# Kernel tuning notes

Hardware: AMD Instinct MI355X
Metric: run time of the kernel (lower is better)

Reference implementation:

```python
import jax, jax.numpy as jnp
import numpy as np
from jax import lax

INPUT_SIZE, HIDDEN, LAYERS, OUT = 49, 32, 2, 10
B, T = 512, 1024


def _param(key, shape, fan):
    bound = 1.0 / np.sqrt(fan)
    return jax.random.uniform(key, shape, jnp.float32, -bound, bound)


def setup_inputs() -> dict:
    key = jax.random.key(0)
    ks = jax.random.split(key, 12)
    return {
        "x": jax.random.normal(ks[0], (B, T, INPUT_SIZE), jnp.float32),
        "W_ih0": _param(ks[1], (4 * HIDDEN, INPUT_SIZE), HIDDEN),
        "W_hh0": _param(ks[2], (4 * HIDDEN, HIDDEN), HIDDEN),
        "b_ih0": _param(ks[3], (4 * HIDDEN,), HIDDEN),
        "b_hh0": _param(ks[4], (4 * HIDDEN,), HIDDEN),
        "W_ih1": _param(ks[5], (4 * HIDDEN, HIDDEN), HIDDEN),
        "W_hh1": _param(ks[6], (4 * HIDDEN, HIDDEN), HIDDEN),
        "b_ih1": _param(ks[7], (4 * HIDDEN,), HIDDEN),
        "b_hh1": _param(ks[8], (4 * HIDDEN,), HIDDEN),
        "W_out": _param(ks[9], (OUT, HIDDEN), HIDDEN),
        "b_out": _param(ks[10], (OUT,), HIDDEN),
    }


def _lstm_layer(x_tbd, W_ih, W_hh, b_ih, b_hh):
    # x_tbd: [T, B, D]; PyTorch gate order i, f, g, o stacked along 4H.
    H = W_hh.shape[1]
    # Precompute input contribution for all timesteps in one GEMM.
    xg = jnp.einsum('tbd,gd->tbg', x_tbd, W_ih) + b_ih + b_hh  # [T, B, 4H]

    def step(carry, xg_t):
        h, c = carry
        gates = xg_t + h @ W_hh.T  # [B, 4H]
        i, f, g, o = jnp.split(gates, 4, axis=-1)
        i = jax.nn.sigmoid(i)
        f = jax.nn.sigmoid(f)
        g = jnp.tanh(g)
        o = jax.nn.sigmoid(o)
        c = f * c + i * g
        h = o * jnp.tanh(c)
        return (h, c), h

    Bsz = x_tbd.shape[1]
    init = (jnp.zeros((Bsz, H), x_tbd.dtype), jnp.zeros((Bsz, H), x_tbd.dtype))
    _, hs = lax.scan(step, init, xg)
    return hs  # [T, B, H]


def reference(x, W_ih0, W_hh0, b_ih0, b_hh0, W_ih1, W_hh1, b_ih1, b_hh1, W_out, b_out):
    # Eval-mode forward (inter-layer dropout disabled).
    xt = jnp.transpose(x, (1, 0, 2))  # [T, B, 49]
    h0 = _lstm_layer(xt, W_ih0, W_hh0, b_ih0, b_hh0)  # [T, B, 32]
    h1 = _lstm_layer(h0, W_ih1, W_hh1, b_ih1, b_hh1)  # [T, B, 32]
    r_out = jnp.transpose(h1, (1, 0, 2))  # [B, T, 32]
    return r_out @ W_out.T + b_out  # [B, T, 10]
```

## Files before the change

kernel.cpp:

```cpp
#include <hip/hip_runtime.h>
#include <cstddef>

#define TSTEPS 1024
#define NIN    49
#define HID    32
#define OUTD   10
#define XSTR   52
#define NGRP   256

typedef float v2f __attribute__((ext_vector_type(2)));

template<int CTRL>
__device__ __forceinline__ float quad(float v) {
    return __int_as_float(__builtin_amdgcn_mov_dpp(__float_as_int(v), CTRL, 0xF, 0xF, true));
}
__device__ __forceinline__ float sigm(float x) {
    return __builtin_amdgcn_rcpf(1.f + __expf(-x));
}
__device__ __forceinline__ void pkfma(v2f& acc, v2f a, v2f b) {
    asm("v_pk_fma_f32 %0, %1, %2, %0" : "+v"(acc) : "v"(a), "v"(b));
}

__device__ __forceinline__ int ldacq(const int* p) {
    return __hip_atomic_load(p, __ATOMIC_ACQUIRE, __HIP_MEMORY_SCOPE_WORKGROUP);
}
__device__ __forceinline__ void pub(int* p, int v, int lane) {
    if (lane == 0)
        __hip_atomic_store(p, v, __ATOMIC_RELEASE, __HIP_MEMORY_SCOPE_WORKGROUP);
}
__device__ __forceinline__ void waitge(const int* p, int need, int& cache) {
    if (cache >= need) return;
    int c = ldacq(p);
    while (c < need) { __builtin_amdgcn_s_sleep(1); c = ldacq(p); }
    cache = c;
}

#define LOADH2(BASE, H2)                                                     \
    v2f H2[8];                                                               \
    {                                                                        \
        const float4* hp_ = (const float4*)(BASE);                           \
        const float4 a_ = hp_[0], b_ = hp_[1], c_ = hp_[2], d_ = hp_[3];     \
        H2[0] = (v2f){a_.x, a_.y}; H2[1] = (v2f){a_.z, a_.w};                \
        H2[2] = (v2f){b_.x, b_.y}; H2[3] = (v2f){b_.z, b_.w};                \
        H2[4] = (v2f){c_.x, c_.y}; H2[5] = (v2f){c_.z, c_.w};                \
        H2[6] = (v2f){d_.x, d_.y}; H2[7] = (v2f){d_.z, d_.w};                \
    }

#define DOTPK(W2, H2, S0, S1, S2, S3)                                        \
    float S0, S1, S2, S3;                                                    \
    {                                                                        \
        v2f p0 = {0.f,0.f}, p1 = {0.f,0.f}, p2 = {0.f,0.f}, p3 = {0.f,0.f}; \
        _Pragma("unroll")                                                    \
        for (int m_ = 0; m_ < 8; ++m_) {                                     \
            pkfma(p0, W2[0][m_], H2[m_]);                                    \
            pkfma(p1, W2[1][m_], H2[m_]);                                    \
            pkfma(p2, W2[2][m_], H2[m_]);                                    \
            pkfma(p3, W2[3][m_], H2[m_]);                                    \
        }                                                                    \
        S0 = p0.x + p0.y; S1 = p1.x + p1.y;                                  \
        S2 = p2.x + p2.y; S3 = p3.x + p3.y;                                  \
        S0 += quad<0xB1>(S0); S1 += quad<0xB1>(S1);                          \
        S2 += quad<0xB1>(S2); S3 += quad<0xB1>(S3);                          \
    }

__device__ __forceinline__ float gate_act(float s0, float s1, float s2, float s3,
                                          int gp, float& c) {
    const float inA = gp ? s2 + s2 : s0;
    const float inB = gp ? s3 : s1;
    const float sA = sigm(inA);
    const float sB = sigm(inB);
    const float vA = gp ? fmaf(2.f, sA, -1.f) : sA;
    const float xA = quad<0xB1>(vA);
    const float xB = quad<0xB1>(sB);
    const float ig = gp ? xA : vA;
    const float fg = gp ? xB : sB;
    const float gg = gp ? vA : xA;
    const float og = gp ? sB : xB;
    c = fmaf(fg, c, ig * gg);
    return og * fmaf(2.f, sigm(c + c), -1.f);
}

extern "C" __global__ void __launch_bounds__(256, 2)
lstm_async(const float* __restrict__ x,
           const float* __restrict__ Wih0, const float* __restrict__ Whh0,
           const float* __restrict__ bih0, const float* __restrict__ bhh0,
           const float* __restrict__ Wih1, const float* __restrict__ Whh1,
           const float* __restrict__ bih1, const float* __restrict__ bhh1,
           const float* __restrict__ Wout, const float* __restrict__ bout,
           float* __restrict__ y)
{
    const int tid  = threadIdx.x;
    const int wv   = tid >> 6;
    const int lane = tid & 63;

    __shared__ __align__(16) float xs[2 * 16 * XSTR];
    __shared__ __align__(16) float xg0[16][HID][4];
    __shared__ __align__(16) float xg1[16][HID][4];
    __shared__ __align__(16) float h0r[16][HID];
    __shared__ __align__(16) float h1r[16][HID];
    __shared__ int ctr[5];

    {
        float* z0 = &h0r[0][0];
        float* z1 = &h1r[0][0];
        for (int i = tid; i < 16 * HID; i += 256) { z0[i] = 0.f; z1[i] = 0.f; }
        if (tid < 5) ctr[tid] = -1;
    }
    __syncthreads();

    const float* __restrict__ xb = x + (size_t)blockIdx.x * TSTEPS * NIN;
    float* __restrict__ yb       = y + (size_t)blockIdx.x * TSTEPS * OUTD;

    if (wv == 0) {
        const int j = lane >> 1, gp = lane & 1;
        v2f wh0[4][8];
#pragma unroll
        for (int g = 0; g < 4; ++g) {
            const float* wr = Whh0 + (g * HID + j) * HID + 16 * gp;
#pragma unroll
            for (int m = 0; m < 8; ++m) wh0[g][m] = (v2f){wr[2*m], wr[2*m + 1]};
        }
        float c0 = 0.f;
        int cProd = -1, cQd = -1;
        __builtin_amdgcn_s_setprio(1);
        for (int g = 0; g < NGRP; ++g) {
            waitge(&ctr[0], 4 * g + 3, cProd);
            if (g >= 4) waitge(&ctr[2], 4 * g - 13, cQd);
#pragma unroll
            for (int u = 0; u < 4; ++u) {
                const int t = 4 * g + u;
                LOADH2(&h0r[(t + 15) & 15][16 * gp], hv)
                DOTPK(wh0, hv, s0, s1, s2, s3)
                const float4 xg = *(const float4*)&xg0[t & 15][j][0];
                const float hval = gate_act(s0 + xg.x, s1 + xg.y,
                                            s2 + xg.z, s3 + xg.w, gp, c0);
                if (gp == 0) h0r[t & 15][j] = hval;
            }
            pub(&ctr[1], 4 * g + 3, lane);
        }
    } else if (wv == 1) {
        const int j = lane >> 1, gp = lane & 1;
        v2f wi1[4][8];
        float b1v[4];
#pragma unroll
        for (int g = 0; g < 4; ++g) {
            const float* wr = Wih1 + (g * HID + j) * HID + 16 * gp;
#pragma unroll
            for (int m = 0; m < 8; ++m) wi1[g][m] = (v2f){wr[2*m], wr[2*m + 1]};
            b1v[g] = bih1[g * HID + j] + bhh1[g * HID + j];
        }
        float wo[8], bo = 0.f;
        const int po = lane >> 2, kq = lane & 3;
        if (lane < 40) {
#pragma unroll
            for (int m = 0; m < 8; ++m) wo[m] = Wout[po * HID + kq * 8 + m];
            bo = bout[po];
        } else {
#pragma unroll
            for (int m = 0; m < 8; ++m) wo[m] = 0.f;
        }
        int cL0 = -1, cL1b = -1, cL1d = -1;
        for (int g = 0; g < NGRP + 2; ++g) {
            if (g < NGRP) {
                waitge(&ctr[1], 4 * g + 3, cL0);
                if (g >= 4) waitge(&ctr[3], 4 * g - 13, cL1b);
#pragma unroll
                for (int u = 0; u < 4; ++u) {
                    const int t = 4 * g + u;
                    LOADH2(&h0r[t & 15][16 * gp], hq)
                    DOTPK(wi1, hq, q0, q1, q2, q3)
                    if (gp == 0) {
                        float4 o;
                        o.x = q0 + b1v[0]; o.y = q1 + b1v[1];
                        o.z = q2 + b1v[2]; o.w = q3 + b1v[3];
                        *(float4*)&xg1[t & 15][j][0] = o;
                    }
                }
                pub(&ctr[2], 4 * g + 3, lane);
            }
            if (g >= 2) {
                const int gy = g - 2;
                waitge(&ctr[3], 4 * gy + 3, cL1d);
#pragma unroll
                for (int u = 0; u < 4; ++u) {
                    const int ty = 4 * gy + u;
                    const float* hb = &h1r[ty & 15][kq * 8];
                    const float4 va = *(const float4*)hb;
                    const float4 vb = *(const float4*)(hb + 4);
                    float acc = wo[0]*va.x + wo[1]*va.y + wo[2]*va.z + wo[3]*va.w
                              + wo[4]*vb.x + wo[5]*vb.y + wo[6]*vb.z + wo[7]*vb.w;
                    acc += quad<0xB1>(acc);
                    acc += quad<0x4E>(acc);
                    if (lane < 40 && kq == 0) yb[(size_t)ty * OUTD + po] = acc + bo;
                }
                pub(&ctr[4], 4 * gy + 3, lane);
            }
        }
    } else if (wv == 2) {
        const int j = lane >> 1, gp = lane & 1;
        v2f wh1[4][8];
#pragma unroll
        for (int g = 0; g < 4; ++g) {
            const float* wr = Whh1 + (g * HID + j) * HID + 16 * gp;
#pragma unroll
            for (int m = 0; m < 8; ++m) wh1[g][m] = (v2f){wr[2*m], wr[2*m + 1]};
        }
        float c1 = 0.f;
        int cQd = -1, cPrj = -1;
        __builtin_amdgcn_s_setprio(1);
        for (int g = 0; g < NGRP; ++g) {
            waitge(&ctr[2], 4 * g + 3, cQd);
            if (g >= 4) waitge(&ctr[4], 4 * g - 13, cPrj);
#pragma unroll
            for (int u = 0; u < 4; ++u) {
                const int t = 4 * g + u;
                LOADH2(&h1r[(t + 15) & 15][16 * gp], hv)
                DOTPK(wh1, hv, s0, s1, s2, s3)
                const float4 xg = *(const float4*)&xg1[t & 15][j][0];
                const float hval = gate_act(s0 + xg.x, s1 + xg.y,
                                            s2 + xg.z, s3 + xg.w, gp, c1);
                if (gp == 0) h1r[t & 15][j] = hval;
            }
            pub(&ctr[3], 4 * g + 3, lane);
        }
    } else {
        const int jj = lane & 31;
        const int gA = lane >> 5;
        const int gB = 2 + (lane >> 5);

        v2f wa2[24], wb2[24];
        float wa48, wb48, b0a, b0b;
        {
            const float* wra = Wih0 + (gA * HID + jj) * NIN;
            const float* wrb = Wih0 + (gB * HID + jj) * NIN;
#pragma unroll
            for (int m = 0; m < 24; ++m) {
                wa2[m] = (v2f){wra[2*m], wra[2*m + 1]};
                wb2[m] = (v2f){wrb[2*m], wrb[2*m + 1]};
            }
            wa48 = wra[48]; wb48 = wrb[48];
            b0a = bih0[gA * HID + jj] + bhh0[gA * HID + jj];
            b0b = bih0[gB * HID + jj] + bhh0[gB * HID + jj];
        }

        int laddr[13];
#pragma unroll
        for (int r = 0; r < 13; ++r) {
            const int idx = lane + r * 64;
            const int s_  = idx / NIN;
            laddr[r] = s_ * XSTR + (idx - s_ * NIN);
        }
        float xr[13];

        auto issue = [&](int cn) {
            const float* src = xb + (size_t)cn * 16 * NIN;
#pragma unroll
            for (int r = 0; r < 12; ++r) xr[r] = src[lane + r * 64];
            if (lane < 16) xr[12] = src[lane + 768];
        };
        auto drain = [&](int cn) {
            float* dst = &xs[(cn & 1) * (16 * XSTR)];
#pragma unroll
            for (int r = 0; r < 12; ++r) dst[laddr[r]] = xr[r];
            if (lane < 16) dst[laddr[12]] = xr[12];
        };
        auto pdot = [&](int t) {
            const float* xp = &xs[((t >> 4) & 1) * (16 * XSTR) + (t & 15) * XSTR];
            const float4* x4 = (const float4*)xp;
            v2f aA0 = (v2f){b0a, 0.f}, aA1 = (v2f){0.f, 0.f};
            v2f aB0 = (v2f){b0b, 0.f}, aB1 = (v2f){0.f, 0.f};
#pragma unroll
            for (int u = 0; u < 12; ++u) {
                const float4 xv = x4[u];
                const v2f xlo = (v2f){xv.x, xv.y};
                const v2f xhi = (v2f){xv.z, xv.w};
                pkfma(aA0, wa2[2*u],     xlo);
                pkfma(aA1, wa2[2*u + 1], xhi);
                pkfma(aB0, wb2[2*u],     xlo);
                pkfma(aB1, wb2[2*u + 1], xhi);
            }
            const float x48 = xp[48];
            const float a0 = fmaf(wa48, x48, (aA0.x + aA0.y) + (aA1.x + aA1.y));
            const float a2 = fmaf(wb48, x48, (aB0.x + aB0.y) + (aB1.x + aB1.y));
            xg0[t & 15][jj][gA] = a0;
            xg0[t & 15][jj][gB] = a2;
        };

        issue(0);
        drain(0);

        int cL0 = -1;
        for (int g = 0; g < NGRP; ++g) {
            if (g >= 4) waitge(&ctr[1], 4 * g - 13, cL0);
            const int cn = (g >> 2) + 1;
            if ((g & 3) == 0 && cn < 64) issue(cn);
            pdot(4 * g); pdot(4 * g + 1); pdot(4 * g + 2); pdot(4 * g + 3);
            if ((g & 3) == 2 && cn < 64) drain(cn);
            pub(&ctr[0], 4 * g + 3, lane);
        }
    }
}

extern "C" void kernel_launch(void* const* d_in, const int* in_sizes, int n_in,
                              void* d_out, int out_size, void* d_ws, size_t ws_size,
                              hipStream_t stream) {
    (void)in_sizes; (void)n_in; (void)d_ws; (void)ws_size; (void)out_size;
    const float* x    = (const float*)d_in[0];
    const float* Wih0 = (const float*)d_in[1];
    const float* Whh0 = (const float*)d_in[2];
    const float* bih0 = (const float*)d_in[3];
    const float* bhh0 = (const float*)d_in[4];
    const float* Wih1 = (const float*)d_in[5];
    const float* Whh1 = (const float*)d_in[6];
    const float* bih1 = (const float*)d_in[7];
    const float* bhh1 = (const float*)d_in[8];
    const float* Wout = (const float*)d_in[9];
    const float* bout = (const float*)d_in[10];
    float* y = (float*)d_out;

    lstm_async<<<dim3(512), dim3(256), 0, stream>>>(
        x, Wih0, Whh0, bih0, bhh0, Wih1, Whh1, bih1, bhh1, Wout, bout, y);
}
```

Baseline: 400.3 us.

## Deepen LDS ring buffers to 32 slots and poll counters once per 16 steps

The ring buffers for gate inputs and hidden states grow from 16 to 32 timesteps. Every stage now polls its producer and consumer counters only once every four groups, waiting 16 steps ahead, which cuts spin-wait and acquire-load overhead on the serial recurrence. The projection now trails layer 1 by eight groups and gets a separate drain loop. Wave-to-role mapping is swapped between neighbouring blocks so the two blocks sharing a CU put their critical recurrences on different SIMDs. A small select is dropped in the gate activation. The costs are more LDS per block and coarser, longer producer/consumer latency at the pipeline edges.

```diff
diff --git a/kernel.cpp b/kernel.cpp
--- a/kernel.cpp
+++ b/kernel.cpp
@@ -7,6 +7,7 @@
 #define OUTD   10
 #define XSTR   52
 #define NGRP   256
+#define RMASK  31
 
 typedef float v2f __attribute__((ext_vector_type(2)));
 
@@ -72,16 +73,14 @@
     const float vA = gp ? fmaf(2.f, sA, -1.f) : sA;
     const float xA = quad<0xB1>(vA);
     const float xB = quad<0xB1>(sB);
-    const float ig = gp ? xA : vA;
     const float fg = gp ? xB : sB;
-    const float gg = gp ? vA : xA;
     const float og = gp ? sB : xB;
-    c = fmaf(fg, c, ig * gg);
+    c = fmaf(fg, c, vA * xA);
     return og * fmaf(2.f, sigm(c + c), -1.f);
 }
 
 extern "C" __global__ void __launch_bounds__(256, 2)
-lstm_async(const float* __restrict__ x,
+lstm_amort(const float* __restrict__ x,
            const float* __restrict__ Wih0, const float* __restrict__ Whh0,
            const float* __restrict__ bih0, const float* __restrict__ bhh0,
            const float* __restrict__ Wih1, const float* __restrict__ Whh1,
@@ -90,20 +89,21 @@
            float* __restrict__ y)
 {
     const int tid  = threadIdx.x;
-    const int wv   = tid >> 6;
     const int lane = tid & 63;
+    const int p    = (blockIdx.x ^ (blockIdx.x >> 8)) & 1;
+    const int role = (tid >> 6) ^ p;
 
     __shared__ __align__(16) float xs[2 * 16 * XSTR];
-    __shared__ __align__(16) float xg0[16][HID][4];
-    __shared__ __align__(16) float xg1[16][HID][4];
-    __shared__ __align__(16) float h0r[16][HID];
-    __shared__ __align__(16) float h1r[16][HID];
+    __shared__ __align__(16) float xg0[32][HID][4];
+    __shared__ __align__(16) float xg1[32][HID][4];
+    __shared__ __align__(16) float h0r[32][HID];
+    __shared__ __align__(16) float h1r[32][HID];
     __shared__ int ctr[5];
 
     {
         float* z0 = &h0r[0][0];
         float* z1 = &h1r[0][0];
-        for (int i = tid; i < 16 * HID; i += 256) { z0[i] = 0.f; z1[i] = 0.f; }
+        for (int i = tid; i < 32 * HID; i += 256) { z0[i] = 0.f; z1[i] = 0.f; }
         if (tid < 5) ctr[tid] = -1;
     }
     __syncthreads();
@@ -111,7 +111,7 @@
     const float* __restrict__ xb = x + (size_t)blockIdx.x * TSTEPS * NIN;
     float* __restrict__ yb       = y + (size_t)blockIdx.x * TSTEPS * OUTD;
 
-    if (wv == 0) {
+    if (role == 0) {
         const int j = lane >> 1, gp = lane & 1;
         v2f wh0[4][8];
 #pragma unroll
@@ -124,21 +124,23 @@
         int cProd = -1, cQd = -1;
         __builtin_amdgcn_s_setprio(1);
         for (int g = 0; g < NGRP; ++g) {
-            waitge(&ctr[0], 4 * g + 3, cProd);
-            if (g >= 4) waitge(&ctr[2], 4 * g - 13, cQd);
+            if ((g & 3) == 0) {
+                waitge(&ctr[0], 4 * g + 15, cProd);
+                if (g >= 8) waitge(&ctr[2], 4 * g - 17, cQd);
+            }
 #pragma unroll
             for (int u = 0; u < 4; ++u) {
                 const int t = 4 * g + u;
-                LOADH2(&h0r[(t + 15) & 15][16 * gp], hv)
+                LOADH2(&h0r[(t + RMASK) & RMASK][16 * gp], hv)
                 DOTPK(wh0, hv, s0, s1, s2, s3)
-                const float4 xg = *(const float4*)&xg0[t & 15][j][0];
+                const float4 xg = *(const float4*)&xg0[t & RMASK][j][0];
                 const float hval = gate_act(s0 + xg.x, s1 + xg.y,
                                             s2 + xg.z, s3 + xg.w, gp, c0);
-                if (gp == 0) h0r[t & 15][j] = hval;
+                if (gp == 0) h0r[t & RMASK][j] = hval;
             }
             pub(&ctr[1], 4 * g + 3, lane);
         }
-    } else if (wv == 1) {
+    } else if (role == 1) {
         const int j = lane >> 1, gp = lane & 1;
         v2f wi1[4][8];
         float b1v[4];
@@ -159,32 +161,31 @@
 #pragma unroll
             for (int m = 0; m < 8; ++m) wo[m] = 0.f;
         }
-        int cL0 = -1, cL1b = -1, cL1d = -1;
-        for (int g = 0; g < NGRP + 2; ++g) {
-            if (g < NGRP) {
-                waitge(&ctr[1], 4 * g + 3, cL0);
-                if (g >= 4) waitge(&ctr[3], 4 * g - 13, cL1b);
-#pragma unroll
-                for (int u = 0; u < 4; ++u) {
-                    const int t = 4 * g + u;
-                    LOADH2(&h0r[t & 15][16 * gp], hq)
-                    DOTPK(wi1, hq, q0, q1, q2, q3)
-                    if (gp == 0) {
-                        float4 o;
-                        o.x = q0 + b1v[0]; o.y = q1 + b1v[1];
-                        o.z = q2 + b1v[2]; o.w = q3 + b1v[3];
-                        *(float4*)&xg1[t & 15][j][0] = o;
-                    }
+        int cL0 = -1, cL1 = -1;
+        for (int g = 0; g < NGRP; ++g) {
+            if ((g & 3) == 0) {
+                waitge(&ctr[1], 4 * g + 15, cL0);
+                if (g >= 8) waitge(&ctr[3], 4 * g - 17, cL1);
+            }
+#pragma unroll
+            for (int u = 0; u < 4; ++u) {
+                const int t = 4 * g + u;
+                LOADH2(&h0r[t & RMASK][16 * gp], hq)
+                DOTPK(wi1, hq, q0, q1, q2, q3)
+                if (gp == 0) {
+                    float4 o;
+                    o.x = q0 + b1v[0]; o.y = q1 + b1v[1];
+                    o.z = q2 + b1v[2]; o.w = q3 + b1v[3];
+                    *(float4*)&xg1[t & RMASK][j][0] = o;
                 }
-                pub(&ctr[2], 4 * g + 3, lane);
-            }
-            if (g >= 2) {
-                const int gy = g - 2;
-                waitge(&ctr[3], 4 * gy + 3, cL1d);
+            }
+            pub(&ctr[2], 4 * g + 3, lane);
+            if (g >= 8) {
+                const int gy = g - 8;
 #pragma unroll
                 for (int u = 0; u < 4; ++u) {
                     const int ty = 4 * gy + u;
-                    const float* hb = &h1r[ty & 15][kq * 8];
+                    const float* hb = &h1r[ty & RMASK][kq * 8];
                     const float4 va = *(const float4*)hb;
                     const float4 vb = *(const float4*)(hb + 4);
                     float acc = wo[0]*va.x + wo[1]*va.y + wo[2]*va.z + wo[3]*va.w
@@ -196,7 +197,23 @@
                 pub(&ctr[4], 4 * gy + 3, lane);
             }
         }
-    } else if (wv == 2) {
+        for (int gy = NGRP - 8; gy < NGRP; ++gy) {
+            waitge(&ctr[3], 4 * gy + 3, cL1);
+#pragma unroll
+            for (int u = 0; u < 4; ++u) {
+                const int ty = 4 * gy + u;
+                const float* hb = &h1r[ty & RMASK][kq * 8];
+                const float4 va = *(const float4*)hb;
+                const float4 vb = *(const float4*)(hb + 4);
+                float acc = wo[0]*va.x + wo[1]*va.y + wo[2]*va.z + wo[3]*va.w
+                          + wo[4]*vb.x + wo[5]*vb.y + wo[6]*vb.z + wo[7]*vb.w;
+                acc += quad<0xB1>(acc);
+                acc += quad<0x4E>(acc);
+                if (lane < 40 && kq == 0) yb[(size_t)ty * OUTD + po] = acc + bo;
+            }
+            pub(&ctr[4], 4 * gy + 3, lane);
+        }
+    } else if (role == 2) {
         const int j = lane >> 1, gp = lane & 1;
         v2f wh1[4][8];
 #pragma unroll
@@ -209,17 +226,19 @@
         int cQd = -1, cPrj = -1;
         __builtin_amdgcn_s_setprio(1);
         for (int g = 0; g < NGRP; ++g) {
-            waitge(&ctr[2], 4 * g + 3, cQd);
-            if (g >= 4) waitge(&ctr[4], 4 * g - 13, cPrj);
+            if ((g & 3) == 0) {
+                waitge(&ctr[2], 4 * g + 15, cQd);
+                if (g >= 8) waitge(&ctr[4], 4 * g - 17, cPrj);
+            }
 #pragma unroll
             for (int u = 0; u < 4; ++u) {
                 const int t = 4 * g + u;
-                LOADH2(&h1r[(t + 15) & 15][16 * gp], hv)
+                LOADH2(&h1r[(t + RMASK) & RMASK][16 * gp], hv)
                 DOTPK(wh1, hv, s0, s1, s2, s3)
-                const float4 xg = *(const float4*)&xg1[t & 15][j][0];
+                const float4 xg = *(const float4*)&xg1[t & RMASK][j][0];
                 const float hval = gate_act(s0 + xg.x, s1 + xg.y,
                                             s2 + xg.z, s3 + xg.w, gp, c1);
-                if (gp == 0) h1r[t & 15][j] = hval;
+                if (gp == 0) h1r[t & RMASK][j] = hval;
             }
             pub(&ctr[3], 4 * g + 3, lane);
         }
@@ -282,8 +301,8 @@
             const float x48 = xp[48];
             const float a0 = fmaf(wa48, x48, (aA0.x + aA0.y) + (aA1.x + aA1.y));
             const float a2 = fmaf(wb48, x48, (aB0.x + aB0.y) + (aB1.x + aB1.y));
-            xg0[t & 15][jj][gA] = a0;
-            xg0[t & 15][jj][gB] = a2;
+            xg0[t & RMASK][jj][gA] = a0;
+            xg0[t & RMASK][jj][gB] = a2;
         };
 
         issue(0);
@@ -291,7 +310,8 @@
 
         int cL0 = -1;
         for (int g = 0; g < NGRP; ++g) {
-            if (g >= 4) waitge(&ctr[1], 4 * g - 13, cL0);
+            if ((g & 3) == 0 && g >= 8)
+                waitge(&ctr[1], 4 * g - 17, cL0);
             const int cn = (g >> 2) + 1;
             if ((g & 3) == 0 && cn < 64) issue(cn);
             pdot(4 * g); pdot(4 * g + 1); pdot(4 * g + 2); pdot(4 * g + 3);
@@ -318,6 +338,6 @@
     const float* bout = (const float*)d_in[10];
     float* y = (float*)d_out;
 
-    lstm_async<<<dim3(512), dim3(256), 0, stream>>>(
+    lstm_amort<<<dim3(512), dim3(256), 0, stream>>>(
         x, Wih0, Whh0, bih0, bhh0, Wih1, Whh1, bih1, bhh1, Wout, bout, y);
 }
```

Result: no change. 395.5 us (-1.2%).

## Merge both LSTM recurrences into one wave with layer-1 skewed by lag

Applied to the files above, without the earlier changes.

The layer-0 and layer-1 recurrent steps now run in a single wavefront, with layer 1 trailing by four groups. Their independent dot products and gate math are interleaved so each hides the other's latency. The block shrinks from four waves to three, and counter waits are batched to every other group. This cuts the latency-bound serial chains and inter-wave handoffs, but the merged wave needs twice as many weight registers, and the lag plus the coarser waits could stall the producer waves on the ring buffers.

```diff
diff --git a/kernel.cpp b/kernel.cpp
--- a/kernel.cpp
+++ b/kernel.cpp
@@ -7,6 +7,9 @@
 #define OUTD   10
 #define XSTR   52
 #define NGRP   256
+#define RMASK  15
+#define CMAX   1023
+#define LAG    4
 
 typedef float v2f __attribute__((ext_vector_type(2)));
 
@@ -20,6 +23,7 @@
 __device__ __forceinline__ void pkfma(v2f& acc, v2f a, v2f b) {
     asm("v_pk_fma_f32 %0, %1, %2, %0" : "+v"(acc) : "v"(a), "v"(b));
 }
+__device__ __forceinline__ int imin(int a, int b) { return a < b ? a : b; }
 
 __device__ __forceinline__ int ldacq(const int* p) {
     return __hip_atomic_load(p, __ATOMIC_ACQUIRE, __HIP_MEMORY_SCOPE_WORKGROUP);
@@ -63,6 +67,28 @@
         S2 += quad<0xB1>(S2); S3 += quad<0xB1>(S3);                          \
     }
 
+#define DOTPK2W(WA, WB, HA, HB, A0,A1,A2,A3, B0,B1,B2,B3)                    \
+    float A0,A1,A2,A3,B0,B1,B2,B3;                                           \
+    {                                                                        \
+        v2f pa0={0.f,0.f}, pa1={0.f,0.f}, pa2={0.f,0.f}, pa3={0.f,0.f};      \
+        v2f pb0={0.f,0.f}, pb1={0.f,0.f}, pb2={0.f,0.f}, pb3={0.f,0.f};      \
+        _Pragma("unroll")                                                    \
+        for (int m_ = 0; m_ < 8; ++m_) {                                     \
+            pkfma(pa0, WA[0][m_], HA[m_]); pkfma(pb0, WB[0][m_], HB[m_]);    \
+            pkfma(pa1, WA[1][m_], HA[m_]); pkfma(pb1, WB[1][m_], HB[m_]);    \
+            pkfma(pa2, WA[2][m_], HA[m_]); pkfma(pb2, WB[2][m_], HB[m_]);    \
+            pkfma(pa3, WA[3][m_], HA[m_]); pkfma(pb3, WB[3][m_], HB[m_]);    \
+        }                                                                    \
+        A0 = pa0.x + pa0.y; A1 = pa1.x + pa1.y;                              \
+        A2 = pa2.x + pa2.y; A3 = pa3.x + pa3.y;                              \
+        B0 = pb0.x + pb0.y; B1 = pb1.x + pb1.y;                              \
+        B2 = pb2.x + pb2.y; B3 = pb3.x + pb3.y;                              \
+        A0 += quad<0xB1>(A0); A1 += quad<0xB1>(A1);                          \
+        A2 += quad<0xB1>(A2); A3 += quad<0xB1>(A3);                          \
+        B0 += quad<0xB1>(B0); B1 += quad<0xB1>(B1);                          \
+        B2 += quad<0xB1>(B2); B3 += quad<0xB1>(B3);                          \
+    }
+
 __device__ __forceinline__ float gate_act(float s0, float s1, float s2, float s3,
                                           int gp, float& c) {
     const float inA = gp ? s2 + s2 : s0;
@@ -72,26 +98,24 @@
     const float vA = gp ? fmaf(2.f, sA, -1.f) : sA;
     const float xA = quad<0xB1>(vA);
     const float xB = quad<0xB1>(sB);
-    const float ig = gp ? xA : vA;
     const float fg = gp ? xB : sB;
-    const float gg = gp ? vA : xA;
     const float og = gp ? sB : xB;
-    c = fmaf(fg, c, ig * gg);
+    c = fmaf(fg, c, vA * xA);
     return og * fmaf(2.f, sigm(c + c), -1.f);
 }
 
-extern "C" __global__ void __launch_bounds__(256, 2)
-lstm_async(const float* __restrict__ x,
-           const float* __restrict__ Wih0, const float* __restrict__ Whh0,
-           const float* __restrict__ bih0, const float* __restrict__ bhh0,
-           const float* __restrict__ Wih1, const float* __restrict__ Whh1,
-           const float* __restrict__ bih1, const float* __restrict__ bhh1,
-           const float* __restrict__ Wout, const float* __restrict__ bout,
-           float* __restrict__ y)
+extern "C" __global__ void __launch_bounds__(192, 2)
+lstm_dual(const float* __restrict__ x,
+          const float* __restrict__ Wih0, const float* __restrict__ Whh0,
+          const float* __restrict__ bih0, const float* __restrict__ bhh0,
+          const float* __restrict__ Wih1, const float* __restrict__ Whh1,
+          const float* __restrict__ bih1, const float* __restrict__ bhh1,
+          const float* __restrict__ Wout, const float* __restrict__ bout,
+          float* __restrict__ y)
 {
     const int tid  = threadIdx.x;
-    const int wv   = tid >> 6;
     const int lane = tid & 63;
+    const int w    = tid >> 6;
 
     __shared__ __align__(16) float xs[2 * 16 * XSTR];
     __shared__ __align__(16) float xg0[16][HID][4];
@@ -103,7 +127,7 @@
     {
         float* z0 = &h0r[0][0];
         float* z1 = &h1r[0][0];
-        for (int i = tid; i < 16 * HID; i += 256) { z0[i] = 0.f; z1[i] = 0.f; }
+        for (int i = tid; i < 16 * HID; i += 192) { z0[i] = 0.f; z1[i] = 0.f; }
         if (tid < 5) ctr[tid] = -1;
     }
     __syncthreads();
@@ -111,34 +135,76 @@
     const float* __restrict__ xb = x + (size_t)blockIdx.x * TSTEPS * NIN;
     float* __restrict__ yb       = y + (size_t)blockIdx.x * TSTEPS * OUTD;
 
-    if (wv == 0) {
+    if (w == 0) {
         const int j = lane >> 1, gp = lane & 1;
-        v2f wh0[4][8];
+        v2f wh0[4][8], wh1[4][8];
 #pragma unroll
         for (int g = 0; g < 4; ++g) {
-            const float* wr = Whh0 + (g * HID + j) * HID + 16 * gp;
-#pragma unroll
-            for (int m = 0; m < 8; ++m) wh0[g][m] = (v2f){wr[2*m], wr[2*m + 1]};
-        }
-        float c0 = 0.f;
-        int cProd = -1, cQd = -1;
+            const float* wr0 = Whh0 + (g * HID + j) * HID + 16 * gp;
+            const float* wr1 = Whh1 + (g * HID + j) * HID + 16 * gp;
+#pragma unroll
+            for (int m = 0; m < 8; ++m) {
+                wh0[g][m] = (v2f){wr0[2*m], wr0[2*m + 1]};
+                wh1[g][m] = (v2f){wr1[2*m], wr1[2*m + 1]};
+            }
+        }
+        float c0 = 0.f, c1 = 0.f;
+        int cProd = -1, cQd = -1, cPrj = -1;
         __builtin_amdgcn_s_setprio(1);
-        for (int g = 0; g < NGRP; ++g) {
-            waitge(&ctr[0], 4 * g + 3, cProd);
-            if (g >= 4) waitge(&ctr[2], 4 * g - 13, cQd);
-#pragma unroll
-            for (int u = 0; u < 4; ++u) {
-                const int t = 4 * g + u;
-                LOADH2(&h0r[(t + 15) & 15][16 * gp], hv)
-                DOTPK(wh0, hv, s0, s1, s2, s3)
-                const float4 xg = *(const float4*)&xg0[t & 15][j][0];
-                const float hval = gate_act(s0 + xg.x, s1 + xg.y,
-                                            s2 + xg.z, s3 + xg.w, gp, c0);
-                if (gp == 0) h0r[t & 15][j] = hval;
-            }
-            pub(&ctr[1], 4 * g + 3, lane);
-        }
-    } else if (wv == 1) {
+        for (int g = 0; g < NGRP + LAG; ++g) {
+            if ((g & 1) == 0) {
+                if (g < NGRP) waitge(&ctr[0], imin(4 * g + 7, CMAX), cProd);
+                if (g >= LAG) waitge(&ctr[2], imin(4 * g - 9, CMAX), cQd);
+                if (g >= 8)   waitge(&ctr[4], imin(4 * g - 25, CMAX), cPrj);
+            }
+            if (g >= LAG && g < NGRP) {
+#pragma unroll
+                for (int u = 0; u < 4; ++u) {
+                    const int t0 = 4 * g + u;
+                    const int t1 = t0 - 4 * LAG;
+                    LOADH2(&h0r[(t0 + RMASK) & RMASK][16 * gp], hva)
+                    LOADH2(&h1r[(t1 + RMASK) & RMASK][16 * gp], hvb)
+                    const float4 xga = *(const float4*)&xg0[t0 & RMASK][j][0];
+                    const float4 xgb = *(const float4*)&xg1[t1 & RMASK][j][0];
+                    DOTPK2W(wh0, wh1, hva, hvb, a0, a1, a2, a3, b0, b1, b2, b3)
+                    const float ha = gate_act(a0 + xga.x, a1 + xga.y,
+                                              a2 + xga.z, a3 + xga.w, gp, c0);
+                    const float hb = gate_act(b0 + xgb.x, b1 + xgb.y,
+                                              b2 + xgb.z, b3 + xgb.w, gp, c1);
+                    if (gp == 0) {
+                        h0r[t0 & RMASK][j] = ha;
+                        h1r[t1 & RMASK][j] = hb;
+                    }
+                }
+                pub(&ctr[1], 4 * g + 3, lane);
+                pub(&ctr[3], 4 * (g - LAG) + 3, lane);
+            } else if (g < NGRP) {
+#pragma unroll
+                for (int u = 0; u < 4; ++u) {
+                    const int t0 = 4 * g + u;
+                    LOADH2(&h0r[(t0 + RMASK) & RMASK][16 * gp], hva)
+                    const float4 xga = *(const float4*)&xg0[t0 & RMASK][j][0];
+                    DOTPK(wh0, hva, a0, a1, a2, a3)
+                    const float ha = gate_act(a0 + xga.x, a1 + xga.y,
+                                              a2 + xga.z, a3 + xga.w, gp, c0);
+                    if (gp == 0) h0r[t0 & RMASK][j] = ha;
+                }
+                pub(&ctr[1], 4 * g + 3, lane);
+            } else {
+#pragma unroll
+                for (int u = 0; u < 4; ++u) {
+                    const int t1 = 4 * (g - LAG) + u;
+                    LOADH2(&h1r[(t1 + RMASK) & RMASK][16 * gp], hvb)
+                    const float4 xgb = *(const float4*)&xg1[t1 & RMASK][j][0];
+                    DOTPK(wh1, hvb, b0, b1, b2, b3)
+                    const float hb = gate_act(b0 + xgb.x, b1 + xgb.y,
+                                              b2 + xgb.z, b3 + xgb.w, gp, c1);
+                    if (gp == 0) h1r[t1 & RMASK][j] = hb;
+                }
+                pub(&ctr[3], 4 * (g - LAG) + 3, lane);
+            }
+        }
+    } else if (w == 1) {
         const int j = lane >> 1, gp = lane & 1;
         v2f wi1[4][8];
         float b1v[4];
@@ -159,32 +225,33 @@
 #pragma unroll
             for (int m = 0; m < 8; ++m) wo[m] = 0.f;
         }
-        int cL0 = -1, cL1b = -1, cL1d = -1;
-        for (int g = 0; g < NGRP + 2; ++g) {
+        int cL0 = -1, cL1 = -1;
+        for (int g = 0; g < NGRP + 4; ++g) {
+            if ((g & 1) == 0) {
+                if (g < NGRP) waitge(&ctr[1], imin(4 * g + 7, CMAX), cL0);
+                if (g >= 4)   waitge(&ctr[3], imin(4 * g - 9, CMAX), cL1);
+            }
             if (g < NGRP) {
-                waitge(&ctr[1], 4 * g + 3, cL0);
-                if (g >= 4) waitge(&ctr[3], 4 * g - 13, cL1b);
 #pragma unroll
                 for (int u = 0; u < 4; ++u) {
                     const int t = 4 * g + u;
-                    LOADH2(&h0r[t & 15][16 * gp], hq)
+                    LOADH2(&h0r[t & RMASK][16 * gp], hq)
                     DOTPK(wi1, hq, q0, q1, q2, q3)
                     if (gp == 0) {
                         float4 o;
                         o.x = q0 + b1v[0]; o.y = q1 + b1v[1];
                         o.z = q2 + b1v[2]; o.w = q3 + b1v[3];
-                        *(float4*)&xg1[t & 15][j][0] = o;
+                        *(float4*)&xg1[t & RMASK][j][0] = o;
                     }
                 }
                 pub(&ctr[2], 4 * g + 3, lane);
             }
-            if (g >= 2) {
-                const int gy = g - 2;
-                waitge(&ctr[3], 4 * gy + 3, cL1d);
+            if (g >= 4) {
+                const int gy = g - 4;
 #pragma unroll
                 for (int u = 0; u < 4; ++u) {
                     const int ty = 4 * gy + u;
-                    const float* hb = &h1r[ty & 15][kq * 8];
+                    const float* hb = &h1r[ty & RMASK][kq * 8];
                     const float4 va = *(const float4*)hb;
                     const float4 vb = *(const float4*)(hb + 4);
                     float acc = wo[0]*va.x + wo[1]*va.y + wo[2]*va.z + wo[3]*va.w
@@ -196,38 +263,10 @@
                 pub(&ctr[4], 4 * gy + 3, lane);
             }
         }
-    } else if (wv == 2) {
-        const int j = lane >> 1, gp = lane & 1;
-        v2f wh1[4][8];
-#pragma unroll
-        for (int g = 0; g < 4; ++g) {
-            const float* wr = Whh1 + (g * HID + j) * HID + 16 * gp;
-#pragma unroll
-            for (int m = 0; m < 8; ++m) wh1[g][m] = (v2f){wr[2*m], wr[2*m + 1]};
-        }
-        float c1 = 0.f;
-        int cQd = -1, cPrj = -1;
-        __builtin_amdgcn_s_setprio(1);
-        for (int g = 0; g < NGRP; ++g) {
-            waitge(&ctr[2], 4 * g + 3, cQd);
-            if (g >= 4) waitge(&ctr[4], 4 * g - 13, cPrj);
-#pragma unroll
-            for (int u = 0; u < 4; ++u) {
-                const int t = 4 * g + u;
-                LOADH2(&h1r[(t + 15) & 15][16 * gp], hv)
-                DOTPK(wh1, hv, s0, s1, s2, s3)
-                const float4 xg = *(const float4*)&xg1[t & 15][j][0];
-                const float hval = gate_act(s0 + xg.x, s1 + xg.y,
-                                            s2 + xg.z, s3 + xg.w, gp, c1);
-                if (gp == 0) h1r[t & 15][j] = hval;
-            }
-            pub(&ctr[3], 4 * g + 3, lane);
-        }
     } else {
         const int jj = lane & 31;
         const int gA = lane >> 5;
         const int gB = 2 + (lane >> 5);
-
         v2f wa2[24], wb2[24];
         float wa48, wb48, b0a, b0b;
         {
@@ -282,8 +321,8 @@
             const float x48 = xp[48];
             const float a0 = fmaf(wa48, x48, (aA0.x + aA0.y) + (aA1.x + aA1.y));
             const float a2 = fmaf(wb48, x48, (aB0.x + aB0.y) + (aB1.x + aB1.y));
-            xg0[t & 15][jj][gA] = a0;
-            xg0[t & 15][jj][gB] = a2;
+            xg0[t & RMASK][jj][gA] = a0;
+            xg0[t & RMASK][jj][gB] = a2;
         };
 
         issue(0);
@@ -291,7 +330,8 @@
 
         int cL0 = -1;
         for (int g = 0; g < NGRP; ++g) {
-            if (g >= 4) waitge(&ctr[1], 4 * g - 13, cL0);
+            if ((g & 1) == 0 && g >= 4)
+                waitge(&ctr[1], imin(4 * g - 9, CMAX), cL0);
             const int cn = (g >> 2) + 1;
             if ((g & 3) == 0 && cn < 64) issue(cn);
             pdot(4 * g); pdot(4 * g + 1); pdot(4 * g + 2); pdot(4 * g + 3);
@@ -318,6 +358,6 @@
     const float* bout = (const float*)d_in[10];
     float* y = (float*)d_out;
 
-    lstm_async<<<dim3(512), dim3(256), 0, stream>>>(
+    lstm_dual<<<dim3(512), dim3(192), 0, stream>>>(
         x, Wih0, Whh0, bih0, bhh0, Wih1, Whh1, bih1, bhh1, Wout, bout, y);
 }
```

Result: slower. 474.1 us (+18.4%).
